# Kernel optimization log

Measured on AMD Instinct MI355X. Metric: run time of the kernel, lower is better.

The kernel has to match this reference:

```python
import jax, jax.numpy as jnp
import numpy as np

B, S, D, H = 1, 4096, 768, 12
Dh = D // H  # 64


def setup_inputs() -> dict:
    key = jax.random.key(0)
    ks = jax.random.split(key, 11)
    w = lambda k, sh: jax.random.normal(k, sh, jnp.float32) * 0.02
    return {
        "query": jax.random.normal(ks[0], (B, S, D), jnp.float32),
        "key": jax.random.normal(ks[1], (B, S, D), jnp.float32),
        "value": jax.random.normal(ks[2], (B, S, D), jnp.float32),
        "mask": jnp.ones((B, S), jnp.int32),  # nonzero = attend; mask==0 positions are filled with -inf
        "Wq": w(ks[3], (D, D)), "bq": w(ks[4], (D,)),
        "Wk": w(ks[5], (D, D)), "bk": w(ks[6], (D,)),
        "Wv": w(ks[7], (D, D)), "bv": w(ks[8], (D,)),
        "Wo": w(ks[9], (D, D)), "bo": w(ks[10], (D,)),
    }


def reference(query, key, value, mask, Wq, bq, Wk, bk, Wv, bv, Wo, bo):
    # shape(): (B, S, D) -> (B, H, S, Dh)
    def split_heads(x):
        return x.reshape(B, S, H, Dh).transpose(0, 2, 1, 3)

    q = split_heads(query @ Wq.T + bq) / np.sqrt(Dh).astype(np.float32)
    k = split_heads(key @ Wk.T + bk)
    # multi_rand_attn_cuda is an unbiased randomized estimator of
    # weights @ v_lin(value); the exact-math baseline applies v_lin then
    # contracts with the attention weights per head.
    v = split_heads(value @ Wv.T + bv)

    scores = jnp.einsum('bhqd,bhkd->bhqk', q, k)  # (B,H,S,S)
    scores = jnp.where((mask == 0)[:, None, None, :], -jnp.inf, scores)
    weights = jax.nn.softmax(scores, axis=-1)  # dropout is identity at eval

    ctx = jnp.einsum('bhqk,bhkd->bhqd', weights, v)
    ctx = ctx.transpose(0, 2, 1, 3).reshape(B, S, D)  # unshape
    return ctx @ Wo.T + bo
```

## Files before the change

### kernel.cpp

```cpp
#include <hip/hip_runtime.h>

#define S_LEN 4096
#define D_MODEL 768
#define N_HEADS 12
#define D_HEAD 64

typedef short bf16x8 __attribute__((ext_vector_type(8)));
typedef float f32x4 __attribute__((ext_vector_type(4)));
typedef float f32x16 __attribute__((ext_vector_type(16)));
typedef float f32x4v __attribute__((ext_vector_type(4)));
typedef unsigned short u16;
typedef unsigned short u16x8 __attribute__((ext_vector_type(8)));
typedef unsigned int u32;

__device__ __forceinline__ u16 f2bf(float f) {
  unsigned u = __float_as_uint(f);
  u += 0x7FFFu + ((u >> 16) & 1u);
  return (u16)(u >> 16);
}

__device__ __forceinline__ u32 pk2bf(float lo, float hi) {
  u32 a = __float_as_uint(hi) + 0x8000u;
  u32 b = __float_as_uint(lo) + 0x8000u;
  return __builtin_amdgcn_perm(a, b, 0x07060302u);
}

__device__ __forceinline__ void gl_lds16(const void* g, void* l) {
  __builtin_amdgcn_global_load_lds(
      (const __attribute__((address_space(1))) void*)g,
      (__attribute__((address_space(3))) void*)l, 16, 0, 0);
}

struct CvtArgs {
  const float* s[4];
  u16* d[4];
};

__global__ __launch_bounds__(256) void cvt8_kernel(CvtArgs a, long n) {
  const float* s = a.s[blockIdx.z];
  u16* d = a.d[blockIdx.z];
  long i = ((long)blockIdx.x * 256 + threadIdx.x) * 8;
  if (i >= n) return;
  f32x4v v0 = *(const f32x4v*)(s + i);
  f32x4v v1 = *(const f32x4v*)(s + i + 4);
  u16x8 o;
#pragma unroll
  for (int j = 0; j < 4; ++j) { o[j] = f2bf(v0[j]); o[j + 4] = f2bf(v1[j]); }
  *(u16x8*)(d + i) = o;
}

struct ProjArgs {
  const u16* A[3];
  const u16* W[3];
  const float* bias[3];
  void* out[3];
  float scale[3];
  int mode[3];
};

template <int TM>
__global__ __launch_bounds__(256, TM == 128 ? 2 : 4) void proj_kernel(ProjArgs args) {
  constexpr int MF = TM / 32;
  constexpr int CA = TM / 16;
  const int z = blockIdx.z;
  const u16* __restrict__ A = args.A[z];
  const u16* __restrict__ W = args.W[z];
  const float* __restrict__ bias = args.bias[z];
  const float scale = args.scale[z];
  const int mode = args.mode[z];

  __shared__ u16 Al[TM * 32];
  __shared__ u16 Bl[128 * 32];

  const int tid = threadIdx.x;
  const int w = tid >> 6, l = tid & 63;
  const int l15 = l & 15, quad = l >> 4;
  const int m0 = blockIdx.x * TM;
  const int n0 = blockIdx.y * 128;
  const int wm = (w & 1) * (TM / 2), wn = (w >> 1) * 64;
  const int crow = l >> 2, ccol = (l & 3) * 8;

  f32x4 acc[MF][4] = {};

  for (int kt = 0; kt < 24; ++kt) {
    const int k0 = kt * 32;
#pragma unroll
    for (int i = 0; i < CA / 4; ++i) {
      const int sub = w * (CA / 4) + i;
      const int row = sub * 16 + crow;
      gl_lds16(&A[(size_t)(m0 + row) * D_MODEL + k0 + ccol], &Al[sub * 512 + l * 8]);
    }
#pragma unroll
    for (int i = 0; i < 2; ++i) {
      const int sub = w * 2 + i;
      const int row = sub * 16 + crow;
      gl_lds16(&W[(size_t)(n0 + row) * D_MODEL + k0 + ccol], &Bl[sub * 512 + l * 8]);
    }
    __syncthreads();
    bf16x8 af[MF], bfr[4];
#pragma unroll
    for (int mf = 0; mf < MF; ++mf)
      af[mf] = *(const bf16x8*)&Al[(wm + mf * 16 + l15) * 32 + quad * 8];
#pragma unroll
    for (int nf = 0; nf < 4; ++nf)
      bfr[nf] = *(const bf16x8*)&Bl[(wn + nf * 16 + l15) * 32 + quad * 8];
#pragma unroll
    for (int mf = 0; mf < MF; ++mf)
#pragma unroll
      for (int nf = 0; nf < 4; ++nf)
        acc[mf][nf] = __builtin_amdgcn_mfma_f32_16x16x32_bf16(af[mf], bfr[nf], acc[mf][nf], 0, 0, 0);
    __syncthreads();
  }

#pragma unroll
  for (int nf = 0; nf < 4; ++nf) {
    const int col = n0 + wn + nf * 16 + l15;
    const float bv = bias[col];
#pragma unroll
    for (int mf = 0; mf < MF; ++mf) {
#pragma unroll
      for (int r = 0; r < 4; ++r) {
        const int row = m0 + wm + mf * 16 + quad * 4 + r;
        const float v = (acc[mf][nf][r] + bv) * scale;
        if (mode == 0) {
          ((u16*)args.out[z])[(size_t)row * D_MODEL + col] = f2bf(v);
        } else if (mode == 2) {
          ((float*)args.out[z])[(size_t)row * D_MODEL + col] = v;
        } else if (mode == 3) {
          const int hh = col >> 6, d = col & 63;
          const int st = row >> 5, kl = row & 31;
          const int s = d >> 4, gg = (d >> 3) & 1, j = d & 7;
          ((u16*)args.out[z])[(size_t)((hh * 128 + st) * 4 + s) * 512 + (gg * 32 + kl) * 8 + j] = f2bf(v);
        } else {
          const int hh = col >> 6, d = col & 63;
          const int st = row >> 5, r16 = row & 15, u = (row >> 4) & 1;
          const int j = (r16 & 3) | (((r16 >> 3) & 1) << 2);
          const int gg = (r16 >> 2) & 1;
          const int db = (d >> 5) & 1, vl = d & 31;
          ((u16*)args.out[z])[(size_t)((hh * 128 + st) * 4 + db * 2 + u) * 512 + (gg * 32 + vl) * 8 + j] = f2bf(v);
        }
      }
    }
  }
}

__global__ __launch_bounds__(256, 3) void flash_kernel(
    const u16* __restrict__ Qb, const u16* __restrict__ Kpk,
    const u16* __restrict__ Vpk, const int* __restrict__ mask,
    u16* __restrict__ Ctx) {
  __shared__ char smem[33792];

  const int tid = threadIdx.x;
  const int w = tid >> 6, l = tid & 63;
  const int l31 = l & 31, g = l >> 5;
  const int a = w & 1, b = w >> 1;
  const int h = blockIdx.y;
  const int q0 = blockIdx.x * 64 + a * 32;

  bf16x8 qf[4];
  {
    const u16* qrow = Qb + (size_t)(q0 + l31) * D_MODEL + h * D_HEAD + g * 8;
#pragma unroll
    for (int s = 0; s < 4; ++s) qf[s] = *(const bf16x8*)(qrow + s * 16);
  }

  const char* kvg = a ? (const char*)(Vpk + ((size_t)h * 128 + b * 64) * 2048)
                      : (const char*)(Kpk + ((size_t)h * 128 + b * 64) * 2048);
  char* pair = smem + b * 16384;
  const int akv = a * 4096;
  const size_t lo = (size_t)l * 16;

  f32x16 oacc0 = {}, oacc1 = {};
  float lsum = 0.f;
  int mv[2];

  mv[0] = mask[b * 2048 + l31];
#pragma unroll
  for (int c = 0; c < 4; ++c) gl_lds16(kvg + c * 1024 + lo, pair + akv + c * 1024);

  int buf = 0;
  for (int it = 0; it < 64; ++it) {
    __syncthreads();
    const unsigned long long mb = __ballot(mv[buf] != 0);
    const char* cb = pair + buf * 8192;
    bf16x8 kf[4], vf[4];
#pragma unroll
    for (int c = 0; c < 4; ++c) kf[c] = *(const bf16x8*)(cb + c * 1024 + lo);
#pragma unroll
    for (int c = 0; c < 4; ++c) vf[c] = *(const bf16x8*)(cb + 4096 + c * 1024 + lo);

    if (it < 63) {
      mv[buf ^ 1] = mask[(b * 64 + it + 1) * 32 + l31];
      char* nb = pair + (buf ^ 1) * 8192 + akv;
      const char* src = kvg + (size_t)(it + 1) * 4096;
#pragma unroll
      for (int c = 0; c < 4; ++c) gl_lds16(src + c * 1024 + lo, nb + c * 1024);
    }

    f32x16 sacc = {};
#pragma unroll
    for (int s = 0; s < 4; ++s)
      sacc = __builtin_amdgcn_mfma_f32_32x32x16_bf16(kf[s], qf[s], sacc, 0, 0, 0);

#pragma unroll
    for (int r = 0; r < 16; ++r) sacc[r] = __builtin_amdgcn_exp2f(sacc[r]);
    if (mb + 1ull != 0ull) {
      const unsigned mh = (unsigned)(mb >> (4 * g));
#pragma unroll
      for (int r = 0; r < 16; ++r)
        if (!((mh >> ((r & 3) + 8 * (r >> 2))) & 1u)) sacc[r] = 0.f;
    }
    float ts = 0.f;
#pragma unroll
    for (int r = 0; r < 16; ++r) ts += sacc[r];
    lsum += ts;

    u32 pk[8];
#pragma unroll
    for (int i = 0; i < 8; ++i) pk[i] = pk2bf(sacc[2 * i], sacc[2 * i + 1]);
#pragma unroll
    for (int u = 0; u < 2; ++u) {
      union { u32 u4[4]; bf16x8 s; } bp;
#pragma unroll
      for (int i = 0; i < 4; ++i) bp.u4[i] = pk[4 * u + i];
      oacc0 = __builtin_amdgcn_mfma_f32_32x32x16_bf16(vf[u], bp.s, oacc0, 0, 0, 0);
      oacc1 = __builtin_amdgcn_mfma_f32_32x32x16_bf16(vf[2 + u], bp.s, oacc1, 0, 0, 0);
    }
    buf ^= 1;
  }

  __syncthreads();
  float* Ol = (float*)smem;
  float* Ll = (float*)(smem + 32768);
#pragma unroll
  for (int r = 0; r < 16; ++r) {
    Ol[((w * 2 + 0) * 16 + r) * 64 + l] = oacc0[r];
    Ol[((w * 2 + 1) * 16 + r) * 64 + l] = oacc1[r];
  }
  Ll[w * 64 + l] = lsum;
  __syncthreads();

  float Lt = Ll[a * 64 + l] + Ll[a * 64 + (l ^ 32)] +
             Ll[(a + 2) * 64 + l] + Ll[(a + 2) * 64 + (l ^ 32)];
  const float linv = 1.0f / Lt;
#pragma unroll
  for (int rr = 0; rr < 4; ++rr) {
    float v[4];
#pragma unroll
    for (int i = 0; i < 4; ++i) {
      const int r = rr * 4 + i;
      v[i] = (Ol[((a * 2 + b) * 16 + r) * 64 + l] +
              Ol[((a * 2 + 4 + b) * 16 + r) * 64 + l]) * linv;
    }
    u16* cp = Ctx + (size_t)(q0 + l31) * D_MODEL + h * D_HEAD + b * 32 + rr * 8 + 4 * g;
    *(u32*)(cp) = pk2bf(v[0], v[1]);
    *(u32*)(cp + 2) = pk2bf(v[2], v[3]);
  }
}

extern "C" void kernel_launch(void* const* d_in, const int* in_sizes, int n_in,
                              void* d_out, int out_size, void* d_ws, size_t ws_size,
                              hipStream_t stream) {
  const float* query = (const float*)d_in[0];
  const float* key   = (const float*)d_in[1];
  const float* value = (const float*)d_in[2];
  const int*   maskp = (const int*)d_in[3];
  const float* Wq = (const float*)d_in[4];
  const float* bq = (const float*)d_in[5];
  const float* Wk = (const float*)d_in[6];
  const float* bk = (const float*)d_in[7];
  const float* Wv = (const float*)d_in[8];
  const float* bv = (const float*)d_in[9];
  const float* Wo = (const float*)d_in[10];
  const float* bo = (const float*)d_in[11];

  char* ws = (char*)d_ws;
  const size_t SZX = (size_t)S_LEN * D_MODEL * 2;
  const size_t SZW = (size_t)D_MODEL * D_MODEL * 2;
  u16* Xq  = (u16*)(ws);
  u16* Xk  = (u16*)(ws + SZX);
  u16* Xv  = (u16*)(ws + 2 * SZX);
  u16* Qb  = (u16*)(ws + 3 * SZX);
  u16* Kpk = (u16*)(ws + 4 * SZX);
  u16* Vpk = (u16*)(ws + 5 * SZX);
  u16* Wqb = (u16*)(ws + 6 * SZX);
  u16* Wkb = (u16*)(ws + 6 * SZX + SZW);
  u16* Wvb = (u16*)(ws + 6 * SZX + 2 * SZW);
  u16* Wob = (u16*)(ws + 6 * SZX + 3 * SZW);
  u16* Ctx = Xq;

  CvtArgs ca;
  ca.s[0] = query; ca.s[1] = key; ca.s[2] = value; ca.s[3] = query;
  ca.d[0] = Xq;    ca.d[1] = Xk;  ca.d[2] = Xv;    ca.d[3] = Xq;
  cvt8_kernel<<<dim3(1536, 1, 3), 256, 0, stream>>>(ca, (long)S_LEN * D_MODEL);

  CvtArgs cw;
  cw.s[0] = Wq;  cw.s[1] = Wk;  cw.s[2] = Wv;  cw.s[3] = Wo;
  cw.d[0] = Wqb; cw.d[1] = Wkb; cw.d[2] = Wvb; cw.d[3] = Wob;
  cvt8_kernel<<<dim3(288, 1, 4), 256, 0, stream>>>(cw, (long)D_MODEL * D_MODEL);

  ProjArgs pa;
  pa.A[0] = Xq;  pa.A[1] = Xk;  pa.A[2] = Xv;
  pa.W[0] = Wqb; pa.W[1] = Wkb; pa.W[2] = Wvb;
  pa.bias[0] = bq; pa.bias[1] = bk; pa.bias[2] = bv;
  pa.out[0] = Qb; pa.out[1] = Kpk; pa.out[2] = Vpk;
  pa.scale[0] = 0.125f * 1.4426950408889634f; pa.scale[1] = 1.f; pa.scale[2] = 1.f;
  pa.mode[0] = 0; pa.mode[1] = 3; pa.mode[2] = 4;
  proj_kernel<128><<<dim3(32, 6, 3), 256, 0, stream>>>(pa);

  flash_kernel<<<dim3(64, N_HEADS, 1), 256, 0, stream>>>(Qb, Kpk, Vpk, maskp, Ctx);

  ProjArgs po;
  po.A[0] = Ctx; po.A[1] = Ctx; po.A[2] = Ctx;
  po.W[0] = Wob; po.W[1] = Wob; po.W[2] = Wob;
  po.bias[0] = bo; po.bias[1] = bo; po.bias[2] = bo;
  po.out[0] = d_out; po.out[1] = d_out; po.out[2] = d_out;
  po.scale[0] = 1.f; po.scale[1] = 1.f; po.scale[2] = 1.f;
  po.mode[0] = 2; po.mode[1] = 2; po.mode[2] = 2;
  proj_kernel<64><<<dim3(64, 6, 1), 256, 0, stream>>>(po);
}
```

Measured before the change: 218.0 us.

## Split flash attention KV range across waves with register double-buffered global loads

The flash kernel now gives each wave both 32-query halves and a quarter of the key/value sequence. Each wave loads K/V fragments straight from global memory into registers, double-buffered, instead of staging them through LDS with per-iteration block barriers. Partial outputs and row sums are reduced across the four waves through a larger shared buffer at the end. This removes the per-tile __syncthreads and LDS traffic but raises register and LDS use, so occupancy drops from 3 to 2 blocks. The projection kernel also switches to a 64-row tile with twice as many blocks.

New measurement: 220.6 us. About the same (+1.2%).

```diff
diff --git a/kernel.cpp b/kernel.cpp
--- a/kernel.cpp
+++ b/kernel.cpp
@@ -144,104 +144,118 @@
   }
 }
 
-__global__ __launch_bounds__(256, 3) void flash_kernel(
+__global__ __launch_bounds__(256, 2) void flash_kernel(
     const u16* __restrict__ Qb, const u16* __restrict__ Kpk,
     const u16* __restrict__ Vpk, const int* __restrict__ mask,
     u16* __restrict__ Ctx) {
-  __shared__ char smem[33792];
+  __shared__ char smem[67584];
 
   const int tid = threadIdx.x;
   const int w = tid >> 6, l = tid & 63;
   const int l31 = l & 31, g = l >> 5;
-  const int a = w & 1, b = w >> 1;
   const int h = blockIdx.y;
-  const int q0 = blockIdx.x * 64 + a * 32;
-
-  bf16x8 qf[4];
-  {
-    const u16* qrow = Qb + (size_t)(q0 + l31) * D_MODEL + h * D_HEAD + g * 8;
-#pragma unroll
-    for (int s = 0; s < 4; ++s) qf[s] = *(const bf16x8*)(qrow + s * 16);
-  }
-
-  const char* kvg = a ? (const char*)(Vpk + ((size_t)h * 128 + b * 64) * 2048)
-                      : (const char*)(Kpk + ((size_t)h * 128 + b * 64) * 2048);
-  char* pair = smem + b * 16384;
-  const int akv = a * 4096;
-  const size_t lo = (size_t)l * 16;
-
-  f32x16 oacc0 = {}, oacc1 = {};
-  float lsum = 0.f;
-  int mv[2];
-
-  mv[0] = mask[b * 2048 + l31];
-#pragma unroll
-  for (int c = 0; c < 4; ++c) gl_lds16(kvg + c * 1024 + lo, pair + akv + c * 1024);
-
-  int buf = 0;
-  for (int it = 0; it < 64; ++it) {
-    __syncthreads();
-    const unsigned long long mb = __ballot(mv[buf] != 0);
-    const char* cb = pair + buf * 8192;
-    bf16x8 kf[4], vf[4];
-#pragma unroll
-    for (int c = 0; c < 4; ++c) kf[c] = *(const bf16x8*)(cb + c * 1024 + lo);
-#pragma unroll
-    for (int c = 0; c < 4; ++c) vf[c] = *(const bf16x8*)(cb + 4096 + c * 1024 + lo);
-
-    if (it < 63) {
-      mv[buf ^ 1] = mask[(b * 64 + it + 1) * 32 + l31];
-      char* nb = pair + (buf ^ 1) * 8192 + akv;
-      const char* src = kvg + (size_t)(it + 1) * 4096;
-#pragma unroll
-      for (int c = 0; c < 4; ++c) gl_lds16(src + c * 1024 + lo, nb + c * 1024);
-    }
-
-    f32x16 sacc = {};
-#pragma unroll
-    for (int s = 0; s < 4; ++s)
-      sacc = __builtin_amdgcn_mfma_f32_32x32x16_bf16(kf[s], qf[s], sacc, 0, 0, 0);
-
-#pragma unroll
-    for (int r = 0; r < 16; ++r) sacc[r] = __builtin_amdgcn_exp2f(sacc[r]);
-    if (mb + 1ull != 0ull) {
-      const unsigned mh = (unsigned)(mb >> (4 * g));
+  const int q0 = blockIdx.x * 64;
+
+  bf16x8 qf[2][4];
+#pragma unroll
+  for (int qs = 0; qs < 2; ++qs) {
+    const u16* qrow = Qb + (size_t)(q0 + qs * 32 + l31) * D_MODEL + h * D_HEAD + g * 8;
+#pragma unroll
+    for (int s = 0; s < 4; ++s) qf[qs][s] = *(const bf16x8*)(qrow + s * 16);
+  }
+
+  const u16* kb = Kpk + ((size_t)h * 128 + w * 32) * 2048 + l * 8;
+  const u16* vb = Vpk + ((size_t)h * 128 + w * 32) * 2048 + l * 8;
+  const int* mk = mask + w * 1024 + l31;
+
+  f32x16 oacc[2][2] = {};
+  float lsum[2] = {0.f, 0.f};
+
+  bf16x8 kfA[4], vfA[4], kfB[4], vfB[4];
+  int mvA, mvB;
+
+  mvA = mk[0];
+#pragma unroll
+  for (int c = 0; c < 4; ++c) kfA[c] = *(const bf16x8*)(kb + c * 512);
+#pragma unroll
+  for (int c = 0; c < 4; ++c) vfA[c] = *(const bf16x8*)(vb + c * 512);
+
+#define FLASH_COMPUTE(KF, VF, MV)                                              \
+  {                                                                            \
+    const unsigned long long mb = __ballot((MV) != 0);                         \
+    _Pragma("unroll") for (int qs = 0; qs < 2; ++qs) {                         \
+      f32x16 sacc = {};                                                        \
+      _Pragma("unroll") for (int s = 0; s < 4; ++s)                            \
+          sacc = __builtin_amdgcn_mfma_f32_32x32x16_bf16(KF[s], qf[qs][s],     \
+                                                         sacc, 0, 0, 0);       \
+      _Pragma("unroll") for (int r = 0; r < 16; ++r)                           \
+          sacc[r] = __builtin_amdgcn_exp2f(sacc[r]);                           \
+      if (mb + 1ull != 0ull) {                                                 \
+        const unsigned mh = (unsigned)(mb >> (4 * g));                         \
+        _Pragma("unroll") for (int r = 0; r < 16; ++r)                         \
+            if (!((mh >> ((r & 3) + 8 * (r >> 2))) & 1u)) sacc[r] = 0.f;       \
+      }                                                                        \
+      float ts = 0.f;                                                          \
+      _Pragma("unroll") for (int r = 0; r < 16; ++r) ts += sacc[r];            \
+      lsum[qs] += ts;                                                          \
+      u32 pk[8];                                                               \
+      _Pragma("unroll") for (int i = 0; i < 8; ++i)                            \
+          pk[i] = pk2bf(sacc[2 * i], sacc[2 * i + 1]);                         \
+      _Pragma("unroll") for (int u = 0; u < 2; ++u) {                          \
+        union { u32 u4[4]; bf16x8 s; } bp;                                     \
+        _Pragma("unroll") for (int i = 0; i < 4; ++i) bp.u4[i] = pk[4 * u + i];\
+        oacc[qs][0] = __builtin_amdgcn_mfma_f32_32x32x16_bf16(VF[u], bp.s,     \
+                                                              oacc[qs][0], 0, 0, 0); \
+        oacc[qs][1] = __builtin_amdgcn_mfma_f32_32x32x16_bf16(VF[2 + u], bp.s, \
+                                                              oacc[qs][1], 0, 0, 0); \
+      }                                                                        \
+    }                                                                          \
+  }
+
+  for (int p = 0; p < 16; ++p) {
+    {
+      const int nt = 2 * p + 1;
+      mvB = mk[nt * 32];
+      const u16* kn = kb + (size_t)nt * 2048;
+      const u16* vn = vb + (size_t)nt * 2048;
+#pragma unroll
+      for (int c = 0; c < 4; ++c) kfB[c] = *(const bf16x8*)(kn + c * 512);
+#pragma unroll
+      for (int c = 0; c < 4; ++c) vfB[c] = *(const bf16x8*)(vn + c * 512);
+      FLASH_COMPUTE(kfA, vfA, mvA)
+    }
+    {
+      const int nt = (2 * p + 2 < 32) ? 2 * p + 2 : 31;
+      mvA = mk[nt * 32];
+      const u16* kn = kb + (size_t)nt * 2048;
+      const u16* vn = vb + (size_t)nt * 2048;
+#pragma unroll
+      for (int c = 0; c < 4; ++c) kfA[c] = *(const bf16x8*)(kn + c * 512);
+#pragma unroll
+      for (int c = 0; c < 4; ++c) vfA[c] = *(const bf16x8*)(vn + c * 512);
+      FLASH_COMPUTE(kfB, vfB, mvB)
+    }
+  }
+#undef FLASH_COMPUTE
+
+  float* Ol = (float*)smem;
+  float* Ll = (float*)(smem + 65536);
+#pragma unroll
+  for (int qs = 0; qs < 2; ++qs) {
+#pragma unroll
+    for (int db = 0; db < 2; ++db)
 #pragma unroll
       for (int r = 0; r < 16; ++r)
-        if (!((mh >> ((r & 3) + 8 * (r >> 2))) & 1u)) sacc[r] = 0.f;
-    }
-    float ts = 0.f;
-#pragma unroll
-    for (int r = 0; r < 16; ++r) ts += sacc[r];
-    lsum += ts;
-
-    u32 pk[8];
-#pragma unroll
-    for (int i = 0; i < 8; ++i) pk[i] = pk2bf(sacc[2 * i], sacc[2 * i + 1]);
-#pragma unroll
-    for (int u = 0; u < 2; ++u) {
-      union { u32 u4[4]; bf16x8 s; } bp;
-#pragma unroll
-      for (int i = 0; i < 4; ++i) bp.u4[i] = pk[4 * u + i];
-      oacc0 = __builtin_amdgcn_mfma_f32_32x32x16_bf16(vf[u], bp.s, oacc0, 0, 0, 0);
-      oacc1 = __builtin_amdgcn_mfma_f32_32x32x16_bf16(vf[2 + u], bp.s, oacc1, 0, 0, 0);
-    }
-    buf ^= 1;
-  }
-
+        Ol[((w * 4 + qs * 2 + db) * 16 + r) * 64 + l] = oacc[qs][db][r];
+    Ll[w * 128 + qs * 64 + l] = lsum[qs];
+  }
   __syncthreads();
-  float* Ol = (float*)smem;
-  float* Ll = (float*)(smem + 32768);
-#pragma unroll
-  for (int r = 0; r < 16; ++r) {
-    Ol[((w * 2 + 0) * 16 + r) * 64 + l] = oacc0[r];
-    Ol[((w * 2 + 1) * 16 + r) * 64 + l] = oacc1[r];
-  }
-  Ll[w * 64 + l] = lsum;
-  __syncthreads();
-
-  float Lt = Ll[a * 64 + l] + Ll[a * 64 + (l ^ 32)] +
-             Ll[(a + 2) * 64 + l] + Ll[(a + 2) * 64 + (l ^ 32)];
+
+  const int qs = w & 1, db = w >> 1;
+  float Lt = 0.f;
+#pragma unroll
+  for (int kq = 0; kq < 4; ++kq)
+    Lt += Ll[kq * 128 + qs * 64 + l] + Ll[kq * 128 + qs * 64 + (l ^ 32)];
   const float linv = 1.0f / Lt;
 #pragma unroll
   for (int rr = 0; rr < 4; ++rr) {
@@ -249,10 +263,13 @@
 #pragma unroll
     for (int i = 0; i < 4; ++i) {
       const int r = rr * 4 + i;
-      v[i] = (Ol[((a * 2 + b) * 16 + r) * 64 + l] +
-              Ol[((a * 2 + 4 + b) * 16 + r) * 64 + l]) * linv;
-    }
-    u16* cp = Ctx + (size_t)(q0 + l31) * D_MODEL + h * D_HEAD + b * 32 + rr * 8 + 4 * g;
+      float acc = 0.f;
+#pragma unroll
+      for (int kq = 0; kq < 4; ++kq)
+        acc += Ol[((kq * 4 + qs * 2 + db) * 16 + r) * 64 + l];
+      v[i] = acc * linv;
+    }
+    u16* cp = Ctx + (size_t)(q0 + qs * 32 + l31) * D_MODEL + h * D_HEAD + db * 32 + rr * 8 + 4 * g;
     *(u32*)(cp) = pk2bf(v[0], v[1]);
     *(u32*)(cp + 2) = pk2bf(v[2], v[3]);
   }
@@ -306,7 +323,7 @@
   pa.out[0] = Qb; pa.out[1] = Kpk; pa.out[2] = Vpk;
   pa.scale[0] = 0.125f * 1.4426950408889634f; pa.scale[1] = 1.f; pa.scale[2] = 1.f;
   pa.mode[0] = 0; pa.mode[1] = 3; pa.mode[2] = 4;
-  proj_kernel<128><<<dim3(32, 6, 3), 256, 0, stream>>>(pa);
+  proj_kernel<64><<<dim3(64, 6, 3), 256, 0, stream>>>(pa);
 
   flash_kernel<<<dim3(64, N_HEADS, 1), 256, 0, stream>>>(Qb, Kpk, Vpk, maskp, Ctx);
 
```
